# Optimization experiments

Measured on AMD Instinct MI355X. Metric: run time of the kernel, lower is better.

## Reference

```python
import jax, jax.numpy as jnp
import numpy as np

EPS = 1.1920928955078125e-07  # torch fp32 default eps for F.rms_norm
N_HEADS = 16
HEAD_DIM = 128


def apply_rotary_emb(x, cos, sin):
    # x: [B,S,H,D]; cos/sin: [1,S,1,D/2]
    d = x.shape[-1] // 2
    x1, x2 = x[..., :d], x[..., d:]
    return jnp.concatenate([x1 * cos + x2 * sin, -x1 * sin + x2 * cos], axis=-1)


def rms_norm(x):
    # F.rms_norm over last dim, no learned weight
    ms = jnp.mean(jnp.square(x), axis=-1, keepdims=True)
    return x * jax.lax.rsqrt(ms + EPS)


def setup_inputs() -> dict:
    key = jax.random.key(0)
    ks = jax.random.split(key, 7)
    B, S, D = 2, 2048, 2048
    half = HEAD_DIM // 2
    # rotary tables (built like standard RoPE for realism)
    inv_freq = 1.0 / (10000.0 ** (np.arange(0, half, dtype=np.float32) / half))
    t = np.arange(S, dtype=np.float32)
    freqs = np.outer(t, inv_freq)  # [S, D/2]
    cos = jnp.asarray(np.cos(freqs))[None, :, None, :]
    sin = jnp.asarray(np.sin(freqs))[None, :, None, :]
    sd = 1.0 / np.sqrt(D)
    return {
        "x": jax.random.normal(ks[0], (B, S, D), jnp.float32),
        "cos": cos,
        "sin": sin,
        "Wq": jax.random.normal(ks[1], (D, D), jnp.float32) * sd,
        "Wk": jax.random.normal(ks[2], (D, D), jnp.float32) * sd,
        "Wv": jax.random.normal(ks[3], (D, D), jnp.float32) * sd,
        "Wo": jax.random.normal(ks[4], (D, D), jnp.float32) * sd,
    }


def reference(x, cos, sin, Wq, Wk, Wv, Wo):
    B, S, D = x.shape
    H, Hd = N_HEADS, HEAD_DIM
    q = (x @ Wq.T).reshape(B, S, H, Hd)
    k = (x @ Wk.T).reshape(B, S, H, Hd)
    v = (x @ Wv.T).reshape(B, S, H, Hd)
    q = apply_rotary_emb(q, cos[:, :S], sin[:, :S])
    k = apply_rotary_emb(k, cos[:, :S], sin[:, :S])
    q = rms_norm(q) * 1.2  # [B,S,H,Hd]
    k = rms_norm(k) * 1.2
    scale = 1.0 / jnp.sqrt(jnp.asarray(Hd, x.dtype))
    # scores: [B,H,Sq,Sk]
    scores = jnp.einsum("bqhd,bkhd->bhqk", q, k) * scale
    attn = jax.nn.softmax(scores, axis=-1)
    y = jnp.einsum("bhqk,bkhd->bqhd", attn, v).reshape(B, S, D)
    return y @ Wo.T
```

## Files before the change

kernel.cpp:

```cpp
#include <hip/hip_runtime.h>
#include <hip/hip_bf16.h>
#include <math.h>

typedef __bf16 bf16;
typedef __attribute__((ext_vector_type(8))) __bf16 bf16x8;
typedef __attribute__((ext_vector_type(4))) float f32x4;
typedef __attribute__((ext_vector_type(16))) float f32x16;

#define DEV __device__ __forceinline__

DEV void gload16(const void* g, void* l) {
    __builtin_amdgcn_global_load_lds(
        (__attribute__((address_space(1))) void*)(void*)g,
        (__attribute__((address_space(3))) void*)l, 16, 0, 0);
}

DEV unsigned pk2(float a, float b) {
    union { bf16 h[2]; unsigned u; } z;
    z.h[0] = (bf16)a; z.h[1] = (bf16)b;
    return z.u;
}

DEV void plswap(unsigned& a, unsigned& b) {
    asm volatile("v_permlane32_swap_b32 %0, %1" : "+v"(a), "+v"(b));
}

__global__ __launch_bounds__(256) void cvt_kernel(const float* __restrict__ in,
                                                  bf16* __restrict__ out, int n8) {
    for (int i = blockIdx.x * 256 + threadIdx.x; i < n8; i += gridDim.x * 256) {
        const float4* p = (const float4*)(in + (size_t)i * 8);
        float4 a = p[0], b = p[1];
        bf16x8 o;
        o[0] = (bf16)a.x; o[1] = (bf16)a.y; o[2] = (bf16)a.z; o[3] = (bf16)a.w;
        o[4] = (bf16)b.x; o[5] = (bf16)b.y; o[6] = (bf16)b.z; o[7] = (bf16)b.w;
        *(bf16x8*)(out + (size_t)i * 8) = o;
    }
}

template <bool F32OUT>
__global__ __launch_bounds__(256) void gemm_bt(const bf16* __restrict__ A,
                                               const bf16* __restrict__ B,
                                               void* __restrict__ Cout,
                                               int M, int N, int K) {
    __shared__ __align__(16) bf16 As[128 * 64];
    __shared__ __align__(16) bf16 Bs[128 * 64];
    const int tid = threadIdx.x, lane = tid & 63, wv = tid >> 6;
    const int tm = blockIdx.y * 128, tn = blockIdx.x * 128;
    const int wr = (wv >> 1) * 64, wc = (wv & 1) * 64;

    f32x4 acc[4][4] = {};
    const int scb = (lane & 7) * 16;

    for (int k0 = 0; k0 < K; k0 += 64) {
#pragma unroll
        for (int i = 0; i < 4; ++i) {
            int chunk = wv * 4 + i;
            int row = chunk * 8 + (lane >> 3);
            int cb = scb ^ ((row & 7) << 4);
            gload16((const char*)(A + (size_t)(tm + row) * K + k0) + cb,
                    (char*)As + chunk * 1024);
            gload16((const char*)(B + (size_t)(tn + row) * K + k0) + cb,
                    (char*)Bs + chunk * 1024);
        }
        __syncthreads();
#pragma unroll
        for (int kk = 0; kk < 2; ++kk) {
            bf16x8 af[4], bfr[4];
#pragma unroll
            for (int m = 0; m < 4; ++m) {
                int row = wr + m * 16 + (lane & 15);
                int cb = (kk * 64 + ((lane >> 4) * 16)) ^ ((row & 7) << 4);
                af[m] = *(const bf16x8*)((const char*)As + row * 128 + cb);
            }
#pragma unroll
            for (int n = 0; n < 4; ++n) {
                int row = wc + n * 16 + (lane & 15);
                int cb = (kk * 64 + ((lane >> 4) * 16)) ^ ((row & 7) << 4);
                bfr[n] = *(const bf16x8*)((const char*)Bs + row * 128 + cb);
            }
#pragma unroll
            for (int m = 0; m < 4; ++m)
#pragma unroll
                for (int n = 0; n < 4; ++n)
                    acc[m][n] = __builtin_amdgcn_mfma_f32_16x16x32_bf16(
                        af[m], bfr[n], acc[m][n], 0, 0, 0);
        }
        __syncthreads();
    }
#pragma unroll
    for (int m = 0; m < 4; ++m)
#pragma unroll
        for (int n = 0; n < 4; ++n)
#pragma unroll
            for (int r = 0; r < 4; ++r) {
                int row = tm + wr + m * 16 + (lane >> 4) * 4 + r;
                int col = tn + wc + n * 16 + (lane & 15);
                if (F32OUT)
                    ((float*)Cout)[(size_t)row * N + col] = acc[m][n][r];
                else
                    ((bf16*)Cout)[(size_t)row * N + col] = (bf16)acc[m][n][r];
            }
}

__global__ __launch_bounds__(256) void rope_rms(bf16* __restrict__ q,
                                                bf16* __restrict__ k,
                                                const float* __restrict__ cosp,
                                                const float* __restrict__ sinp) {
    int gw = blockIdx.x * 4 + (threadIdx.x >> 6);
    int lane = threadIdx.x & 63;
    bf16* base = (blockIdx.y == 0) ? q : k;
    int m = gw >> 4, h = gw & 15;
    int s = m & 2047;
    bf16* p = base + (size_t)m * 2048 + h * 128;
    float x1 = (float)p[lane], x2 = (float)p[lane + 64];
    float c = cosp[s * 64 + lane], si = sinp[s * 64 + lane];
    float r1 = x1 * c + x2 * si;
    float r2 = x2 * c - x1 * si;
    float ss = r1 * r1 + r2 * r2;
#pragma unroll
    for (int msk = 1; msk < 64; msk <<= 1) ss += __shfl_xor(ss, msk);
    float sc = rsqrtf(ss * (1.0f / 128.0f) + 1.1920928955078125e-07f) * 1.2f;
    if (blockIdx.y == 0) sc *= (0.08838834764831845f * 1.4426950408889634f);
    p[lane] = (bf16)(r1 * sc);
    p[lane + 64] = (bf16)(r2 * sc);
}

__global__ __launch_bounds__(256, 3) void attn_kernel(const bf16* __restrict__ q,
                                                      const bf16* __restrict__ k,
                                                      const bf16* __restrict__ v,
                                                      bf16* __restrict__ y) {
    __shared__ __align__(16) bf16 Ks[64 * 128];
    __shared__ __align__(16) bf16 Vt[128][72];

    const int tid = threadIdx.x, lane = tid & 63, wv = tid >> 6;
    const int q31 = lane & 31, h5 = lane >> 5;

    int wgid = blockIdx.y * 16 + blockIdx.x;
    int xcd = wgid & 7, j = wgid >> 3;
    int bh = xcd * 4 + (j >> 4);
    int qblk = j & 15;
    const int b = bh >> 4, h = bh & 15;
    const int q0 = qblk * 128;

    const bf16* qptr = q + (size_t)(b * 2048 + q0 + wv * 32 + q31) * 2048 +
                       h * 128 + h5 * 8;
    bf16x8 qf[8];
#pragma unroll
    for (int ks = 0; ks < 8; ++ks) qf[ks] = *(const bf16x8*)(qptr + ks * 16);

    float mrun = -INFINITY, lrun = 0.f;
    f32x16 acco[4] = {};

    const bf16* vbase = v + (size_t)(b * 2048 + wv * 16) * 2048 + h * 128 + 2 * lane;
    const bf16* kbase = k + (size_t)(b * 2048) * 2048 + h * 128;

    for (int kt = 0; kt < 2048; kt += 64) {
#pragma unroll
        for (int i = 0; i < 4; ++i) {
            int chunk = wv * 4 + i;
            int row = chunk * 4 + (lane >> 4);
            int cb = ((lane & 15) * 16) ^ ((row & 7) << 4);
            gload16((const char*)(kbase + (size_t)(kt + row) * 2048) + cb,
                    (char*)Ks + chunk * 1024);
        }
        {
            const bf16* vp = vbase + (size_t)kt * 2048;
            unsigned u[16];
#pragma unroll
            for (int jj = 0; jj < 16; ++jj)
                u[jj] = *(const unsigned*)(vp + (size_t)jj * 2048);
            union { unsigned short s[8]; bf16x8 v8; } r0a, r0b, r1a, r1b;
#pragma unroll
            for (int jj = 0; jj < 8; ++jj) {
                r0a.s[jj] = (unsigned short)(u[jj] & 0xffff);
                r1a.s[jj] = (unsigned short)(u[jj] >> 16);
                r0b.s[jj] = (unsigned short)(u[jj + 8] & 0xffff);
                r1b.s[jj] = (unsigned short)(u[jj + 8] >> 16);
            }
            *(bf16x8*)(&Vt[2 * lane][wv * 16]) = r0a.v8;
            *(bf16x8*)(&Vt[2 * lane][wv * 16 + 8]) = r0b.v8;
            *(bf16x8*)(&Vt[2 * lane + 1][wv * 16]) = r1a.v8;
            *(bf16x8*)(&Vt[2 * lane + 1][wv * 16 + 8]) = r1b.v8;
        }
        __syncthreads();

        f32x16 st[2];
        __builtin_amdgcn_s_setprio(1);
#pragma unroll
        for (int kvb = 0; kvb < 2; ++kvb) {
            f32x16 a = {};
#pragma unroll
            for (int ks = 0; ks < 8; ++ks) {
                int row = kvb * 32 + q31;
                int cb = (32 * ks + 16 * h5) ^ ((row & 7) << 4);
                const bf16x8 kf = *(const bf16x8*)((const char*)Ks + row * 256 + cb);
                a = __builtin_amdgcn_mfma_f32_32x32x16_bf16(kf, qf[ks], a, 0, 0, 0);
            }
            st[kvb] = a;
        }
        __builtin_amdgcn_s_setprio(0);

        float t8[8];
#pragma unroll
        for (int r = 0; r < 8; ++r)
            t8[r] = fmaxf(fmaxf(st[0][r], st[0][r + 8]),
                          fmaxf(st[1][r], st[1][r + 8]));
        float mx = fmaxf(fmaxf(fmaxf(t8[0], t8[1]), fmaxf(t8[2], t8[3])),
                         fmaxf(fmaxf(t8[4], t8[5]), fmaxf(t8[6], t8[7])));
        mx = fmaxf(mx, __shfl_xor(mx, 32));

        if (__any(mx - mrun > 8.0f)) {
            float mn = fmaxf(mrun, mx);
            float alpha = exp2f(mrun - mn);
            mrun = mn;
            lrun *= alpha;
#pragma unroll
            for (int r = 0; r < 16; ++r) {
                int qr = (r & 3) + 8 * (r >> 2) + 4 * h5;
                float al = __shfl(alpha, qr);
                acco[0][r] *= al; acco[1][r] *= al;
                acco[2][r] *= al; acco[3][r] *= al;
            }
        }

        unsigned w[2][8];
        float rsa = 0.f, rsb = 0.f;
#pragma unroll
        for (int kvb = 0; kvb < 2; ++kvb)
#pragma unroll
            for (int i = 0; i < 8; ++i) {
                float p0 = exp2f(st[kvb][2 * i] - mrun);
                float p1 = exp2f(st[kvb][2 * i + 1] - mrun);
                if (i & 1) rsb += p0 + p1; else rsa += p0 + p1;
                w[kvb][i] = pk2(p0, p1);
            }
        float rs = rsa + rsb;
        rs += __shfl_xor(rs, 32);
        lrun += rs;

        __builtin_amdgcn_s_setprio(1);
#pragma unroll
        for (int b2 = 0; b2 < 2; ++b2)
#pragma unroll
            for (int ksl = 0; ksl < 2; ++ksl) {
                const int ks = b2 * 2 + ksl, u0 = ksl * 4;
                unsigned f0 = w[b2][u0 + 0], f2 = w[b2][u0 + 2];
                unsigned f1 = w[b2][u0 + 1], f3 = w[b2][u0 + 3];
                plswap(f0, f2);
                plswap(f1, f3);
                union { unsigned uu[4]; bf16x8 v8; } fr;
                fr.uu[0] = f0; fr.uu[1] = f1; fr.uu[2] = f2; fr.uu[3] = f3;
#pragma unroll
                for (int dblk = 0; dblk < 4; ++dblk) {
                    const bf16x8 vf =
                        *(const bf16x8*)(&Vt[dblk * 32 + q31][ks * 16 + h5 * 8]);
                    acco[dblk] = __builtin_amdgcn_mfma_f32_32x32x16_bf16(
                        fr.v8, vf, acco[dblk], 0, 0, 0);
                }
            }
        __builtin_amdgcn_s_setprio(0);
        __syncthreads();
    }

    float linv = 1.0f / lrun;
#pragma unroll
    for (int r = 0; r < 16; ++r) {
        int qr = (r & 3) + 8 * (r >> 2) + 4 * h5;
        float il = __shfl(linv, qr);
        size_t row = (size_t)(b * 2048 + q0 + wv * 32 + qr) * 2048 + h * 128;
#pragma unroll
        for (int dblk = 0; dblk < 4; ++dblk)
            y[row + dblk * 32 + q31] = (bf16)(acco[dblk][r] * il);
    }
}

extern "C" void kernel_launch(void* const* d_in, const int* in_sizes, int n_in,
                              void* d_out, int out_size, void* d_ws, size_t ws_size,
                              hipStream_t stream) {
    const float* x = (const float*)d_in[0];
    const float* cs = (const float*)d_in[1];
    const float* sn = (const float*)d_in[2];
    const float* Wq = (const float*)d_in[3];
    const float* Wk = (const float*)d_in[4];
    const float* Wv = (const float*)d_in[5];
    const float* Wo = (const float*)d_in[6];

    char* ws = (char*)d_ws;
    bf16* xb  = (bf16*)(ws + 0);
    bf16* wqb = (bf16*)(ws + 16777216);
    bf16* wkb = (bf16*)(ws + 25165824);
    bf16* wvb = (bf16*)(ws + 33554432);
    bf16* wob = (bf16*)(ws + 41943040);
    bf16* qb  = (bf16*)(ws + 50331648);
    bf16* kb  = (bf16*)(ws + 67108864);
    bf16* vb  = (bf16*)(ws + 83886080);
    bf16* yb  = (bf16*)(ws + 100663296);

    cvt_kernel<<<1024, 256, 0, stream>>>(x, xb, 8388608 / 8);
    cvt_kernel<<<512, 256, 0, stream>>>(Wq, wqb, 4194304 / 8);
    cvt_kernel<<<512, 256, 0, stream>>>(Wk, wkb, 4194304 / 8);
    cvt_kernel<<<512, 256, 0, stream>>>(Wv, wvb, 4194304 / 8);
    cvt_kernel<<<512, 256, 0, stream>>>(Wo, wob, 4194304 / 8);

    dim3 g(16, 32);
    gemm_bt<false><<<g, 256, 0, stream>>>(xb, wqb, qb, 4096, 2048, 2048);
    gemm_bt<false><<<g, 256, 0, stream>>>(xb, wkb, kb, 4096, 2048, 2048);
    gemm_bt<false><<<g, 256, 0, stream>>>(xb, wvb, vb, 4096, 2048, 2048);

    rope_rms<<<dim3(16384, 2), 256, 0, stream>>>(qb, kb, cs, sn);

    attn_kernel<<<dim3(16, 32), 256, 0, stream>>>(qb, kb, vb, yb);

    gemm_bt<true><<<g, 256, 0, stream>>>(yb, wob, d_out, 4096, 2048, 2048);
}
```

Baseline: 345.2 us.

## Double-buffer K and V tiles in attention to overlap loads with MFMA

```diff
diff --git a/kernel.cpp b/kernel.cpp
--- a/kernel.cpp
+++ b/kernel.cpp
@@ -125,12 +125,12 @@
     p[lane + 64] = (bf16)(r2 * sc);
 }
 
-__global__ __launch_bounds__(256, 3) void attn_kernel(const bf16* __restrict__ q,
+__global__ __launch_bounds__(256, 2) void attn_kernel(const bf16* __restrict__ q,
                                                       const bf16* __restrict__ k,
                                                       const bf16* __restrict__ v,
                                                       bf16* __restrict__ y) {
-    __shared__ __align__(16) bf16 Ks[64 * 128];
-    __shared__ __align__(16) bf16 Vt[128][72];
+    __shared__ __align__(16) bf16 Ks[2][64 * 128];
+    __shared__ __align__(16) bf16 Vt[2][128][72];
 
     const int tid = threadIdx.x, lane = tid & 63, wv = tid >> 6;
     const int q31 = lane & 31, h5 = lane >> 5;
@@ -154,35 +154,50 @@
     const bf16* vbase = v + (size_t)(b * 2048 + wv * 16) * 2048 + h * 128 + 2 * lane;
     const bf16* kbase = k + (size_t)(b * 2048) * 2048 + h * 128;
 
-    for (int kt = 0; kt < 2048; kt += 64) {
+    unsigned u[16];
+
+    auto stageK = [&](int t, int buf) {
 #pragma unroll
         for (int i = 0; i < 4; ++i) {
             int chunk = wv * 4 + i;
             int row = chunk * 4 + (lane >> 4);
             int cb = ((lane & 15) * 16) ^ ((row & 7) << 4);
-            gload16((const char*)(kbase + (size_t)(kt + row) * 2048) + cb,
-                    (char*)Ks + chunk * 1024);
-        }
-        {
-            const bf16* vp = vbase + (size_t)kt * 2048;
-            unsigned u[16];
-#pragma unroll
-            for (int jj = 0; jj < 16; ++jj)
-                u[jj] = *(const unsigned*)(vp + (size_t)jj * 2048);
-            union { unsigned short s[8]; bf16x8 v8; } r0a, r0b, r1a, r1b;
-#pragma unroll
-            for (int jj = 0; jj < 8; ++jj) {
-                r0a.s[jj] = (unsigned short)(u[jj] & 0xffff);
-                r1a.s[jj] = (unsigned short)(u[jj] >> 16);
-                r0b.s[jj] = (unsigned short)(u[jj + 8] & 0xffff);
-                r1b.s[jj] = (unsigned short)(u[jj + 8] >> 16);
-            }
-            *(bf16x8*)(&Vt[2 * lane][wv * 16]) = r0a.v8;
-            *(bf16x8*)(&Vt[2 * lane][wv * 16 + 8]) = r0b.v8;
-            *(bf16x8*)(&Vt[2 * lane + 1][wv * 16]) = r1a.v8;
-            *(bf16x8*)(&Vt[2 * lane + 1][wv * 16 + 8]) = r1b.v8;
-        }
-        __syncthreads();
+            gload16((const char*)(kbase + (size_t)(t * 64 + row) * 2048) + cb,
+                    (char*)(Ks[buf]) + chunk * 1024);
+        }
+    };
+    auto loadV = [&](int t) {
+        const bf16* vp = vbase + (size_t)(t * 64) * 2048;
+#pragma unroll
+        for (int jj = 0; jj < 16; ++jj)
+            u[jj] = *(const unsigned*)(vp + (size_t)jj * 2048);
+    };
+    auto writeV = [&](int buf) {
+        union { unsigned short s[8]; bf16x8 v8; } r0a, r0b, r1a, r1b;
+#pragma unroll
+        for (int jj = 0; jj < 8; ++jj) {
+            r0a.s[jj] = (unsigned short)(u[jj] & 0xffff);
+            r1a.s[jj] = (unsigned short)(u[jj] >> 16);
+            r0b.s[jj] = (unsigned short)(u[jj + 8] & 0xffff);
+            r1b.s[jj] = (unsigned short)(u[jj + 8] >> 16);
+        }
+        *(bf16x8*)(&Vt[buf][2 * lane][wv * 16]) = r0a.v8;
+        *(bf16x8*)(&Vt[buf][2 * lane][wv * 16 + 8]) = r0b.v8;
+        *(bf16x8*)(&Vt[buf][2 * lane + 1][wv * 16]) = r1a.v8;
+        *(bf16x8*)(&Vt[buf][2 * lane + 1][wv * 16 + 8]) = r1b.v8;
+    };
+
+    stageK(0, 0);
+    loadV(0);
+    writeV(0);
+    __syncthreads();
+
+    for (int t = 0; t < 32; ++t) {
+        const int c = t & 1;
+        if (t < 31) {
+            stageK(t + 1, c ^ 1);
+            loadV(t + 1);
+        }
 
         f32x16 st[2];
         __builtin_amdgcn_s_setprio(1);
@@ -193,7 +208,8 @@
             for (int ks = 0; ks < 8; ++ks) {
                 int row = kvb * 32 + q31;
                 int cb = (32 * ks + 16 * h5) ^ ((row & 7) << 4);
-                const bf16x8 kf = *(const bf16x8*)((const char*)Ks + row * 256 + cb);
+                const bf16x8 kf =
+                    *(const bf16x8*)((const char*)(Ks[c]) + row * 256 + cb);
                 a = __builtin_amdgcn_mfma_f32_32x32x16_bf16(kf, qf[ks], a, 0, 0, 0);
             }
             st[kvb] = a;
@@ -252,13 +268,15 @@
                 fr.uu[0] = f0; fr.uu[1] = f1; fr.uu[2] = f2; fr.uu[3] = f3;
 #pragma unroll
                 for (int dblk = 0; dblk < 4; ++dblk) {
-                    const bf16x8 vf =
-                        *(const bf16x8*)(&Vt[dblk * 32 + q31][ks * 16 + h5 * 8]);
+                    const bf16x8 vf = *(const bf16x8*)(
+                        &Vt[c][dblk * 32 + q31][ks * 16 + h5 * 8]);
                     acco[dblk] = __builtin_amdgcn_mfma_f32_32x32x16_bf16(
                         fr.v8, vf, acco[dblk], 0, 0, 0);
                 }
             }
         __builtin_amdgcn_s_setprio(0);
+
+        if (t < 31) writeV(c ^ 1);
         __syncthreads();
     }
 
```

New measurement: 326.7 us. 1.06x faster.
